# Kernel optimization log

Hardware: AMD Instinct MI355X
Metric: run time of the kernel (lower is better)

Reference implementation:

```python
import jax, jax.numpy as jnp
import numpy as np

BINS = 10
MOMENTUM = 0.5


def setup_inputs() -> dict:
    key = jax.random.key(0)
    k1, k2 = jax.random.split(key)
    B, D = 4096, 512
    x = jax.random.normal(k1, (B, D), dtype=jnp.float32)
    targets = jax.random.randint(k2, (B,), 0, 100, dtype=jnp.int64)
    acc_sum = jnp.zeros((BINS,), dtype=jnp.float32)
    return {"x": x, "acc_sum": acc_sum, "targets": targets}


def reference(x, acc_sum, targets):
    bins, momentum = BINS, MOMENTUM
    B = x.shape[0]
    # bin edges: arange(bins+1)/bins, last edge bumped by 1e-6
    edges = jnp.arange(bins + 1, dtype=jnp.float32) / bins
    edges = edges.at[-1].add(1e-6)

    # F.normalize: x / max(||x||_2, 1e-12) row-wise
    norm = jnp.maximum(jnp.linalg.norm(x, axis=1, keepdims=True), 1e-12)
    xn = x / norm
    cos = xn @ xn.T  # [B, B]

    label = (targets[:, None] == targets[None, :]).astype(jnp.float32)  # [B, B]

    g = jnp.abs(cos - label).ravel()  # gradient-density statistic, in [0, 2]
    # bin index i such that edges[i] <= g < edges[i+1]
    idx = jnp.searchsorted(edges, g, side="right") - 1
    valid = (idx >= 0) & (idx < bins)  # g >= edges[-1] falls in no bin -> weight 0

    # fused histogram (replaces the 10-iteration mask loop)
    counts = jnp.bincount(jnp.where(valid, idx, bins), length=bins + 1)[:bins]
    counts = counts.astype(jnp.float32)

    tot = jnp.float32(B * B)
    acc_new = momentum * acc_sum + (1.0 - momentum) * counts  # EMA update (momentum > 0 path)
    w_bin = tot / (acc_new + 1e-6)  # per-bin weight

    weights = jnp.where(valid, w_bin[jnp.clip(idx, 0, bins - 1)], 0.0)
    valid_num = jnp.sum(counts)
    weights = jnp.where(valid_num > 0, weights / valid_num, weights)

    loss = jnp.mean((label.ravel() - cos.ravel()) ** 2 * weights)
    return loss
```

## Files before the change

### kernel.cpp

```cpp
#include <hip/hip_runtime.h>
#include <hip/hip_bf16.h>

typedef __bf16 bf16x8 __attribute__((ext_vector_type(8)));
typedef float f32x4 __attribute__((ext_vector_type(4)));

typedef __attribute__((address_space(1))) void GAS;
typedef __attribute__((address_space(3))) void LAS;
#define GLOAD16(gp, lp) __builtin_amdgcn_global_load_lds((GAS*)(gp), (LAS*)(lp), 16, 0, 0)

#define NB 4096
#define ND 512
#define NKT 24

__global__ __launch_bounds__(256) void nrm_split_k(const float* __restrict__ x,
                                                   __bf16* __restrict__ hi,
                                                   __bf16* __restrict__ lo,
                                                   float* __restrict__ stats) {
    if (blockIdx.x == 0 && threadIdx.x < 20) stats[threadIdx.x] = 0.0f;
    const int wid = threadIdx.x >> 6, lane = threadIdx.x & 63;
    const int row = blockIdx.x * 4 + wid;
    const float4* xr = reinterpret_cast<const float4*>(x + (size_t)row * ND);
    float4 v0 = xr[lane * 2 + 0];
    float4 v1 = xr[lane * 2 + 1];
    float xv[8] = {v0.x, v0.y, v0.z, v0.w, v1.x, v1.y, v1.z, v1.w};
    float ss = 0.0f;
#pragma unroll
    for (int j = 0; j < 8; ++j) ss += xv[j] * xv[j];
#pragma unroll
    for (int off = 32; off > 0; off >>= 1) ss += __shfl_xor(ss, off);
    const float rn = 1.0f / fmaxf(sqrtf(ss), 1e-12f);
    bf16x8 h, l;
#pragma unroll
    for (int j = 0; j < 8; ++j) {
        float xn = xv[j] * rn;
        __bf16 hb = (__bf16)xn;
        h[j] = hb;
        l[j] = (__bf16)(xn - (float)hb);
    }
    reinterpret_cast<bf16x8*>(hi + (size_t)row * ND)[lane] = h;
    reinterpret_cast<bf16x8*>(lo + (size_t)row * ND)[lane] = l;
}

__global__ __launch_bounds__(512, 2) void gemm_stat_k(const __bf16* __restrict__ hi,
                                                      const __bf16* __restrict__ lo,
                                                      const int* __restrict__ targets,
                                                      float* __restrict__ stats) {
    __shared__ __align__(16) __bf16 lds[2][2][2][128 * 64];
    __shared__ int tgtR[256], tgtC[256];
    __shared__ float red_s[8][10], red_c[8][10];

    const int bid = blockIdx.x;
    const int swz = (bid & 7) * 32 + (bid >> 3);
    const int by = swz >> 4, bx = swz & 15;
    const int row0 = by * 256, col0 = bx * 256;
    const int tid = threadIdx.x, lane = tid & 63;
    const int wid = tid >> 6, wr = wid >> 2, wc = wid & 3;

    if (tid < 256) tgtR[tid] = targets[row0 + tid];
    else           tgtC[tid - 256] = targets[col0 + tid - 256];

    const int c0 = tid, c1 = tid + 512;
    const int r0c = c0 >> 3, x0 = ((c0 & 7) ^ (r0c & 7)) * 8;
    const int r1c = c1 >> 3, x1 = ((c1 & 7) ^ (r1c & 7)) * 8;

    auto STAGE = [&](int s) {
        const int kt = s >> 2, h4 = s & 3;
        const int slot = kt & 1, seg = kt >> 3, kcol = (kt & 7) * 64;
        const bool isA = (h4 < 2);
        const int half = h4 & 1;
        const __bf16* mat = isA ? ((seg == 2) ? lo : hi) : ((seg == 1) ? lo : hi);
        const int brow = (isA ? row0 : col0) + half * 128;
        __bf16* ldst = &lds[slot][isA ? 0 : 1][half][0];
        GLOAD16(mat + (size_t)(brow + r0c) * ND + kcol + x0, ldst + c0 * 8);
        GLOAD16(mat + (size_t)(brow + r1c) * ND + kcol + x1, ldst + c1 * 8);
    };

    const f32x4 fzero = {0.0f, 0.0f, 0.0f, 0.0f};
    f32x4 acc[8][4];
#pragma unroll
    for (int a = 0; a < 8; ++a)
#pragma unroll
        for (int n = 0; n < 4; ++n) acc[a][n] = fzero;

    STAGE(0); STAGE(1); STAGE(2); STAGE(3); STAGE(4);
    asm volatile("s_waitcnt vmcnt(2)" ::: "memory");
    __builtin_amdgcn_s_barrier();
    __builtin_amdgcn_sched_barrier(0);

    const int fr = lane & 15, hi16 = lane >> 4;
    const int Bhalf = wc >> 1;

    for (int kt = 0; kt < NKT; ++kt) {
        const int slot = kt & 1;
        const __bf16* lA = &lds[slot][0][0][0];
        const __bf16* lB = &lds[slot][1][Bhalf][0];
#pragma unroll
        for (int f = 0; f < 4; ++f) {
            const int Mh = f >> 1, kh = f & 1;
            bf16x8 af[4], bf[4];
#pragma unroll
            for (int q = 0; q < 4; ++q) {
                const int row = wr * 64 + q * 16 + fr;
                const int cb = (kh * 64 + hi16 * 16) ^ ((row & 7) << 4);
                af[q] = *(const bf16x8*)((const char*)(lA + Mh * 8192) + row * 128 + cb);
            }
#pragma unroll
            for (int n = 0; n < 4; ++n) {
                const int row = (wc & 1) * 64 + n * 16 + fr;
                const int cb = (kh * 64 + hi16 * 16) ^ ((row & 7) << 4);
                bf[n] = *(const bf16x8*)((const char*)lB + row * 128 + cb);
            }
            const int s = 4 * kt + f + 5;
            if (s < 96) STAGE(s);
            __builtin_amdgcn_s_barrier();
            __builtin_amdgcn_sched_barrier(0);
            __builtin_amdgcn_s_setprio(1);
#pragma unroll
            for (int q = 0; q < 4; ++q)
#pragma unroll
                for (int n = 0; n < 4; ++n)
                    acc[Mh * 4 + q][n] = __builtin_amdgcn_mfma_f32_16x16x32_bf16(
                        af[q], bf[n], acc[Mh * 4 + q][n], 0, 0, 0);
            __builtin_amdgcn_s_setprio(0);
            __builtin_amdgcn_sched_barrier(0);
            if (f == 3) {
                if (kt < 22)       asm volatile("s_waitcnt vmcnt(2)" ::: "memory");
                else if (kt == 22) asm volatile("s_waitcnt vmcnt(0)" ::: "memory");
            }
            __builtin_amdgcn_s_barrier();
            __builtin_amdgcn_sched_barrier(0);
        }
    }

    int tcv[4];
#pragma unroll
    for (int n = 0; n < 4; ++n) tcv[n] = tgtC[wc * 64 + n * 16 + fr];

    constexpr float E[11] = {0.0f, 0.1f, 0.2f, 0.3f, 0.4f, 0.5f,
                             0.6f, 0.7f, 0.8f, 0.9f, 1.0f + 1e-6f};
    float sacc[10], cacc[10];
#pragma unroll
    for (int b = 0; b < 10; ++b) { sacc[b] = 0.0f; cacc[b] = 0.0f; }

    const int rB = wr * 64 + hi16 * 4;
#pragma unroll
    for (int a = 0; a < 8; ++a) {
        int trv[4];
#pragma unroll
        for (int r = 0; r < 4; ++r) trv[r] = tgtR[(a >> 2) * 128 + rB + (a & 3) * 16 + r];
#pragma unroll
        for (int n = 0; n < 4; ++n) {
            f32x4 v = acc[a][n];
            const int tc = tcv[n];
#pragma unroll
            for (int r = 0; r < 4; ++r) {
                const float label = (trv[r] == tc) ? 1.0f : 0.0f;
                const float g = fabsf(v[r] - label);
                const float g2 = g * g;
                bool prev = true;
#pragma unroll
                for (int b = 0; b < 10; ++b) {
                    const bool ge = (g >= E[b + 1]);
                    const bool in = prev && (!ge);
                    sacc[b] += in ? g2 : 0.0f;
                    cacc[b] += in ? 1.0f : 0.0f;
                    prev = ge;
                }
            }
        }
    }

#pragma unroll
    for (int b = 0; b < 10; ++b) {
        float sv = sacc[b], cv = cacc[b];
#pragma unroll
        for (int off = 32; off > 0; off >>= 1) {
            sv += __shfl_xor(sv, off);
            cv += __shfl_xor(cv, off);
        }
        if (lane == 0) { red_s[wid][b] = sv; red_c[wid][b] = cv; }
    }
    __syncthreads();
    if (tid < 10) {
        float s = 0.0f, c = 0.0f;
#pragma unroll
        for (int w = 0; w < 8; ++w) { s += red_s[w][tid]; c += red_c[w][tid]; }
        atomicAdd(&stats[tid], s);
        atomicAdd(&stats[10 + tid], c);
    }
}

__global__ void finalize_k(const float* __restrict__ stats,
                           const float* __restrict__ acc_sum,
                           float* __restrict__ out) {
    if (threadIdx.x == 0) {
        const float tot = 16777216.0f;
        double num = 0.0, valid = 0.0;
#pragma unroll
        for (int b = 0; b < 10; ++b) {
            float cnt = stats[10 + b];
            float accn = 0.5f * acc_sum[b] + 0.5f * cnt;
            float w = tot / (accn + 1e-6f);
            num += (double)stats[b] * (double)w;
            valid += (double)cnt;
        }
        out[0] = (valid > 0.0) ? (float)(num / valid / 16777216.0) : 0.0f;
    }
}

extern "C" void kernel_launch(void* const* d_in, const int* in_sizes, int n_in,
                              void* d_out, int out_size, void* d_ws, size_t ws_size,
                              hipStream_t stream) {
    const float* x = (const float*)d_in[0];
    const float* acc_sum = (const float*)d_in[1];
    const int* targets = (const int*)d_in[2];
    float* out = (float*)d_out;

    char* ws = (char*)d_ws;
    const size_t mat_bytes = (size_t)NB * ND * sizeof(__bf16);
    __bf16* hi = (__bf16*)ws;
    __bf16* lo = (__bf16*)(ws + mat_bytes);
    float* stats = (float*)(ws + 2 * mat_bytes);

    nrm_split_k<<<NB / 4, 256, 0, stream>>>(x, hi, lo, stats);
    gemm_stat_k<<<256, 512, 0, stream>>>(hi, lo, targets, stats);
    finalize_k<<<1, 64, 0, stream>>>(stats, acc_sum, out);
}
```

Baseline: 167.7 us.

## Restructure GEMM prefetch pipeline and fold finalize into last-block epilogue

Replaces the staggered 5-stage prefetch with a whole-k-tile-ahead schedule that issues one quarter-stage per sub-step, using different vmcnt wait points. LDS fragment offsets are precomputed once outside the loop, and the sched_barriers are dropped so the compiler can interleave instructions. The separate finalize kernel is removed: a global atomic counter lets the last block compute the loss. This saves one launch but adds a fence and atomic reads at the tail.

```diff
diff --git a/kernel.cpp b/kernel.cpp
--- a/kernel.cpp
+++ b/kernel.cpp
@@ -16,7 +16,7 @@
                                                    __bf16* __restrict__ hi,
                                                    __bf16* __restrict__ lo,
                                                    float* __restrict__ stats) {
-    if (blockIdx.x == 0 && threadIdx.x < 20) stats[threadIdx.x] = 0.0f;
+    if (blockIdx.x == 0 && threadIdx.x < 21) stats[threadIdx.x] = 0.0f;
     const int wid = threadIdx.x >> 6, lane = threadIdx.x & 63;
     const int row = blockIdx.x * 4 + wid;
     const float4* xr = reinterpret_cast<const float4*>(x + (size_t)row * ND);
@@ -44,7 +44,9 @@
 __global__ __launch_bounds__(512, 2) void gemm_stat_k(const __bf16* __restrict__ hi,
                                                       const __bf16* __restrict__ lo,
                                                       const int* __restrict__ targets,
-                                                      float* __restrict__ stats) {
+                                                      const float* __restrict__ acc_sum,
+                                                      float* __restrict__ stats,
+                                                      float* __restrict__ out) {
     __shared__ __align__(16) __bf16 lds[2][2][2][128 * 64];
     __shared__ int tgtR[256], tgtC[256];
     __shared__ float red_s[8][10], red_c[8][10];
@@ -63,17 +65,29 @@
     const int r0c = c0 >> 3, x0 = ((c0 & 7) ^ (r0c & 7)) * 8;
     const int r1c = c1 >> 3, x1 = ((c1 & 7) ^ (r1c & 7)) * 8;
 
-    auto STAGE = [&](int s) {
-        const int kt = s >> 2, h4 = s & 3;
+    auto STAGE = [&](int kt, int h) {
         const int slot = kt & 1, seg = kt >> 3, kcol = (kt & 7) * 64;
-        const bool isA = (h4 < 2);
-        const int half = h4 & 1;
+        const bool isA = (h == 0) || (h == 3);
+        const int half = (h >= 2) ? 1 : 0;
         const __bf16* mat = isA ? ((seg == 2) ? lo : hi) : ((seg == 1) ? lo : hi);
         const int brow = (isA ? row0 : col0) + half * 128;
-        __bf16* ldst = &lds[slot][isA ? 0 : 1][half][0];
-        GLOAD16(mat + (size_t)(brow + r0c) * ND + kcol + x0, ldst + c0 * 8);
-        GLOAD16(mat + (size_t)(brow + r1c) * ND + kcol + x1, ldst + c1 * 8);
+        __bf16* dst = &lds[slot][isA ? 0 : 1][half][0];
+        GLOAD16(mat + (size_t)(brow + r0c) * ND + kcol + x0, dst + c0 * 8);
+        GLOAD16(mat + (size_t)(brow + r1c) * ND + kcol + x1, dst + c1 * 8);
     };
+
+    const int fr = lane & 15, hi16 = lane >> 4;
+    const int Bhalf = wc >> 1;
+    int offA[2][4], offB[2][4];
+#pragma unroll
+    for (int kh = 0; kh < 2; ++kh)
+#pragma unroll
+        for (int q = 0; q < 4; ++q) {
+            const int ra = wr * 64 + q * 16 + fr;
+            offA[kh][q] = ra * 64 + ((kh * 32 + hi16 * 8) ^ ((ra & 7) << 3));
+            const int rb = (wc & 1) * 64 + q * 16 + fr;
+            offB[kh][q] = rb * 64 + ((kh * 32 + hi16 * 8) ^ ((rb & 7) << 3));
+        }
 
     const f32x4 fzero = {0.0f, 0.0f, 0.0f, 0.0f};
     f32x4 acc[8][4];
@@ -82,38 +96,29 @@
 #pragma unroll
         for (int n = 0; n < 4; ++n) acc[a][n] = fzero;
 
-    STAGE(0); STAGE(1); STAGE(2); STAGE(3); STAGE(4);
+    STAGE(0, 0); STAGE(0, 1); STAGE(0, 2); STAGE(0, 3);
     asm volatile("s_waitcnt vmcnt(2)" ::: "memory");
     __builtin_amdgcn_s_barrier();
-    __builtin_amdgcn_sched_barrier(0);
-
-    const int fr = lane & 15, hi16 = lane >> 4;
-    const int Bhalf = wc >> 1;
 
     for (int kt = 0; kt < NKT; ++kt) {
         const int slot = kt & 1;
-        const __bf16* lA = &lds[slot][0][0][0];
-        const __bf16* lB = &lds[slot][1][Bhalf][0];
+        const __bf16* bA0 = &lds[slot][0][0][0];
+        const __bf16* bA1 = &lds[slot][0][1][0];
+        const __bf16* bB  = &lds[slot][1][Bhalf][0];
+        const bool more = (kt + 1 < NKT);
 #pragma unroll
         for (int f = 0; f < 4; ++f) {
             const int Mh = f >> 1, kh = f & 1;
+            if (more) STAGE(kt + 1, f);
+            const __bf16* bA = Mh ? bA1 : bA0;
             bf16x8 af[4], bf[4];
 #pragma unroll
-            for (int q = 0; q < 4; ++q) {
-                const int row = wr * 64 + q * 16 + fr;
-                const int cb = (kh * 64 + hi16 * 16) ^ ((row & 7) << 4);
-                af[q] = *(const bf16x8*)((const char*)(lA + Mh * 8192) + row * 128 + cb);
-            }
-#pragma unroll
-            for (int n = 0; n < 4; ++n) {
-                const int row = (wc & 1) * 64 + n * 16 + fr;
-                const int cb = (kh * 64 + hi16 * 16) ^ ((row & 7) << 4);
-                bf[n] = *(const bf16x8*)((const char*)lB + row * 128 + cb);
-            }
-            const int s = 4 * kt + f + 5;
-            if (s < 96) STAGE(s);
+            for (int q = 0; q < 4; ++q)
+                af[q] = *reinterpret_cast<const bf16x8*>(bA + offA[kh][q]);
+#pragma unroll
+            for (int n = 0; n < 4; ++n)
+                bf[n] = *reinterpret_cast<const bf16x8*>(bB + offB[kh][n]);
             __builtin_amdgcn_s_barrier();
-            __builtin_amdgcn_sched_barrier(0);
             __builtin_amdgcn_s_setprio(1);
 #pragma unroll
             for (int q = 0; q < 4; ++q)
@@ -122,13 +127,14 @@
                     acc[Mh * 4 + q][n] = __builtin_amdgcn_mfma_f32_16x16x32_bf16(
                         af[q], bf[n], acc[Mh * 4 + q][n], 0, 0, 0);
             __builtin_amdgcn_s_setprio(0);
-            __builtin_amdgcn_sched_barrier(0);
-            if (f == 3) {
-                if (kt < 22)       asm volatile("s_waitcnt vmcnt(2)" ::: "memory");
-                else if (kt == 22) asm volatile("s_waitcnt vmcnt(0)" ::: "memory");
+            if (f == 1) {
+                if (more) asm volatile("s_waitcnt vmcnt(4)" ::: "memory");
+                else      asm volatile("s_waitcnt vmcnt(0)" ::: "memory");
+            }
+            if (f == 3 && more) {
+                asm volatile("s_waitcnt vmcnt(2)" ::: "memory");
             }
             __builtin_amdgcn_s_barrier();
-            __builtin_amdgcn_sched_barrier(0);
         }
     }
 
@@ -187,24 +193,27 @@
         for (int w = 0; w < 8; ++w) { s += red_s[w][tid]; c += red_c[w][tid]; }
         atomicAdd(&stats[tid], s);
         atomicAdd(&stats[10 + tid], c);
-    }
-}
-
-__global__ void finalize_k(const float* __restrict__ stats,
-                           const float* __restrict__ acc_sum,
-                           float* __restrict__ out) {
-    if (threadIdx.x == 0) {
-        const float tot = 16777216.0f;
-        double num = 0.0, valid = 0.0;
-#pragma unroll
-        for (int b = 0; b < 10; ++b) {
-            float cnt = stats[10 + b];
-            float accn = 0.5f * acc_sum[b] + 0.5f * cnt;
-            float w = tot / (accn + 1e-6f);
-            num += (double)stats[b] * (double)w;
-            valid += (double)cnt;
-        }
-        out[0] = (valid > 0.0) ? (float)(num / valid / 16777216.0) : 0.0f;
+        __threadfence();
+    }
+    __syncthreads();
+
+    if (tid == 0) {
+        int old = atomicAdd((int*)&stats[20], 1);
+        if (old == 255) {
+            __threadfence();
+            const float tot = 16777216.0f;
+            double num = 0.0, valid = 0.0;
+#pragma unroll
+            for (int b = 0; b < 10; ++b) {
+                float sb = atomicAdd(&stats[b], 0.0f);
+                float cnt = atomicAdd(&stats[10 + b], 0.0f);
+                float accn = 0.5f * acc_sum[b] + 0.5f * cnt;
+                float w = tot / (accn + 1e-6f);
+                num += (double)sb * (double)w;
+                valid += (double)cnt;
+            }
+            out[0] = (valid > 0.0) ? (float)(num / valid / 16777216.0) : 0.0f;
+        }
     }
 }
 
@@ -223,6 +232,5 @@
     float* stats = (float*)(ws + 2 * mat_bytes);
 
     nrm_split_k<<<NB / 4, 256, 0, stream>>>(x, hi, lo, stats);
-    gemm_stat_k<<<256, 512, 0, stream>>>(hi, lo, targets, stats);
-    finalize_k<<<1, 64, 0, stream>>>(stats, acc_sum, out);
+    gemm_stat_k<<<256, 512, 0, stream>>>(hi, lo, targets, acc_sum, stats, out);
 }
```

Measured after the change: 187.8 us. +12.0%, slower.
